# Kernel tuning notes

Measured on AMD Instinct MI355X. Metric: run time of the kernel, lower is better.

## Reference

```python
import jax, jax.numpy as jnp
import numpy as np

NUM_GROUPS = 32
EPS = 1e-6


def setup_inputs() -> dict:
    key = jax.random.key(0)
    ks = jax.random.split(key, 11)
    b, c, h, w = 4, 512, 64, 64
    s = 0.02
    return {
        "x": jax.random.normal(ks[0], (b, c, h, w), dtype=jnp.float32),
        "gn_w": jnp.ones((c,), dtype=jnp.float32),
        "gn_b": jnp.zeros((c,), dtype=jnp.float32),
        "wq": jax.random.normal(ks[1], (c, c), dtype=jnp.float32) * s,
        "bq": jax.random.normal(ks[2], (c,), dtype=jnp.float32) * s,
        "wk": jax.random.normal(ks[3], (c, c), dtype=jnp.float32) * s,
        "bk": jax.random.normal(ks[4], (c,), dtype=jnp.float32) * s,
        "wv": jax.random.normal(ks[5], (c, c), dtype=jnp.float32) * s,
        "bv": jax.random.normal(ks[6], (c,), dtype=jnp.float32) * s,
        "wo": jax.random.normal(ks[7], (c, c), dtype=jnp.float32) * s,
        "bo": jax.random.normal(ks[8], (c,), dtype=jnp.float32) * s,
    }


def _group_norm(x, gamma, beta):
    b, c, h, w = x.shape
    g = NUM_GROUPS
    xg = x.reshape(b, g, c // g, h, w)
    mean = jnp.mean(xg, axis=(2, 3, 4), keepdims=True)
    var = jnp.var(xg, axis=(2, 3, 4), keepdims=True)
    xg = (xg - mean) * jax.lax.rsqrt(var + EPS)
    x = xg.reshape(b, c, h, w)
    return x * gamma[None, :, None, None] + beta[None, :, None, None]


def _conv1x1(x, wmat, bias):
    # x: [b,c,h,w], wmat: [out,in] -> [b,out,h,w]
    return jnp.einsum('bchw,oc->bohw', x, wmat) + bias[None, :, None, None]


def reference(x, gn_w, gn_b, wq, bq, wk, bk, wv, bv, wo, bo):
    b, c, h, w = x.shape
    h_ = _group_norm(x, gn_w, gn_b)
    q = _conv1x1(h_, wq, bq).reshape(b, c, h * w)  # [b,c,hw]
    k = _conv1x1(h_, wk, bk).reshape(b, c, h * w)
    v = _conv1x1(h_, wv, bv).reshape(b, c, h * w)
    scale = float(c) ** (-0.5)
    # scores[b,i,j] = sum_c q[b,c,i] * k[b,c,j]
    scores = jnp.einsum('bci,bcj->bij', q, k) * scale
    attn = jax.nn.softmax(scores, axis=2)  # softmax over j (keys)
    # out[b,c,i] = sum_j v[b,c,j] * attn[b,i,j]
    out = jnp.einsum('bcj,bij->bci', v, attn).reshape(b, c, h, w)
    out = _conv1x1(out, wo, bo)
    return x + out
```

## Files before the change

### kernel.cpp

```cpp
#include <hip/hip_runtime.h>
#include <math.h>

using short8 = __attribute__((ext_vector_type(8))) short;
using f32x4  = __attribute__((ext_vector_type(4))) float;
using llong2 = __attribute__((ext_vector_type(2))) long long;
using i32x8  = __attribute__((ext_vector_type(8))) int;

__device__ __forceinline__ ushort f2bf(float f) {
    union { float f; uint u; } c; c.f = f;
    uint u = c.u;
    uint r = (u + 0x7FFFu + ((u >> 16) & 1u)) >> 16;
    return (ushort)r;
}
__device__ __forceinline__ float bf2f(ushort h) {
    union { uint u; float f; } c; c.u = ((uint)h) << 16;
    return c.f;
}
__device__ __forceinline__ uint pk4_fp8(float a, float b, float c, float d) {
    int v = __builtin_amdgcn_cvt_pk_fp8_f32(a, b, 0, false);
    v = __builtin_amdgcn_cvt_pk_fp8_f32(c, d, v, true);
    return (uint)v;
}
__device__ __forceinline__ unsigned char f2fp8(float x) {
    return (unsigned char)__builtin_amdgcn_cvt_pk_fp8_f32(x, 0.f, 0, false);
}

__device__ __forceinline__ void gload16(const void* g, void* l) {
    __builtin_amdgcn_global_load_lds(
        (const __attribute__((address_space(1))) unsigned int*)g,
        (__attribute__((address_space(3))) unsigned int*)l,
        16, 0, 0);
}

__global__ __launch_bounds__(256) void prep_weights(
    const float* __restrict__ wq, const float* __restrict__ bq,
    const float* __restrict__ wk, const float* __restrict__ bk,
    const float* __restrict__ wv, const float* __restrict__ wo,
    ushort* __restrict__ Wqk, ushort* __restrict__ Wv, ushort* __restrict__ Wo,
    float* __restrict__ bqk, float* __restrict__ stats, float scale)
{
    int idx = blockIdx.x * 256 + threadIdx.x;
    if (idx < 1024 * 512) {
        float v = (idx < 262144) ? wq[idx] * scale : wk[idx - 262144];
        Wqk[idx] = f2bf(v);
    }
    if (idx < 262144) {
        Wv[idx] = f2bf(wv[idx]);
        Wo[idx] = f2bf(wo[idx]);
    }
    if (idx < 1024) bqk[idx] = (idx < 512) ? bq[idx] * scale : bk[idx - 512];
    if (idx < 256) stats[idx] = 0.f;
}

__global__ __launch_bounds__(256) void gn_stats(
    const float* __restrict__ x, float* __restrict__ stats)
{
    int blk = blockIdx.x;
    int grp = blk >> 3, sub = blk & 7;
    const float* xp = x + (size_t)grp * 65536 + sub * 8192;
    int tid = threadIdx.x;

    float s = 0.f, sq = 0.f;
    #pragma unroll
    for (int j = 0; j < 8; ++j) {
        float4 v = *(const float4*)&xp[tid * 4 + j * 1024];
        s  += v.x + v.y + v.z + v.w;
        sq += v.x * v.x + v.y * v.y + v.z * v.z + v.w * v.w;
    }
    #pragma unroll
    for (int off = 32; off; off >>= 1) {
        s  += __shfl_xor(s,  off, 64);
        sq += __shfl_xor(sq, off, 64);
    }
    __shared__ float red[8];
    if ((tid & 63) == 0) { red[(tid >> 6) * 2] = s; red[(tid >> 6) * 2 + 1] = sq; }
    __syncthreads();
    if (tid == 0) {
        atomicAdd(&stats[grp * 2],     red[0] + red[2] + red[4] + red[6]);
        atomicAdd(&stats[grp * 2 + 1], red[1] + red[3] + red[5] + red[7]);
    }
}

__global__ __launch_bounds__(256) void gn_apply(
    const float* __restrict__ x, const float* __restrict__ gamma,
    const float* __restrict__ beta, const float* __restrict__ stats,
    ushort* __restrict__ hnt)
{
    int blk = blockIdx.x;
    int grp = blk >> 4, tile = blk & 15;
    int b = grp >> 5, g = grp & 31;
    const float* xp = x + (size_t)grp * 65536;
    int tid = threadIdx.x;

    float mean = stats[grp * 2] * (1.f / 65536.f);
    float var  = stats[grp * 2 + 1] * (1.f / 65536.f) - mean * mean;
    float rstd = rsqrtf(var + 1e-6f);

    int i0 = tile * 256;
    __shared__ ushort ls[16][256];
    #pragma unroll
    for (int ch = 0; ch < 16; ++ch) {
        float a = rstd * gamma[g * 16 + ch];
        float c = beta[g * 16 + ch] - mean * a;
        ls[ch][tid] = f2bf(xp[ch * 4096 + i0 + tid] * a + c);
    }
    __syncthreads();
    ushort t[16];
    #pragma unroll
    for (int ch = 0; ch < 16; ++ch) t[ch] = ls[ch][tid];
    size_t dst = ((size_t)b * 4096 + i0 + tid) * 512 + g * 16;
    *(uint4*)&hnt[dst]     = *(const uint4*)&t[0];
    *(uint4*)&hnt[dst + 8] = *(const uint4*)&t[8];
}

__global__ __launch_bounds__(256) void softmax_kernel(
    const ushort* __restrict__ S, unsigned char* __restrict__ P8)
{
    size_t row = blockIdx.x;
    const ushort* p = S + row * 4096;
    int tid = threadIdx.x;

    ushort tmp[16];
    *(uint4*)&tmp[0] = *(const uint4*)&p[tid * 16];
    *(uint4*)&tmp[8] = *(const uint4*)&p[tid * 16 + 8];
    float v[16];
    float mx = -1e30f;
    #pragma unroll
    for (int j = 0; j < 16; ++j) { v[j] = bf2f(tmp[j]); mx = fmaxf(mx, v[j]); }
    #pragma unroll
    for (int off = 32; off; off >>= 1) mx = fmaxf(mx, __shfl_xor(mx, off, 64));
    __shared__ float ls[8];
    if ((tid & 63) == 0) ls[tid >> 6] = mx;
    __syncthreads();
    float m4 = fmaxf(fmaxf(ls[0], ls[1]), fmaxf(ls[2], ls[3]));
    float sum = 0.f;
    #pragma unroll
    for (int j = 0; j < 16; ++j) { v[j] = __expf(v[j] - m4); sum += v[j]; }
    #pragma unroll
    for (int off = 32; off; off >>= 1) sum += __shfl_xor(sum, off, 64);
    if ((tid & 63) == 0) ls[4 + (tid >> 6)] = sum;
    __syncthreads();
    float inv = 256.0f / (ls[4] + ls[5] + ls[6] + ls[7]);
    size_t base = row * 4096 + (size_t)tid * 16;
    uint2 o0, o1;
    o0.x = pk4_fp8(v[0] * inv,  v[1] * inv,  v[2] * inv,  v[3] * inv);
    o0.y = pk4_fp8(v[4] * inv,  v[5] * inv,  v[6] * inv,  v[7] * inv);
    o1.x = pk4_fp8(v[8] * inv,  v[9] * inv,  v[10] * inv, v[11] * inv);
    o1.y = pk4_fp8(v[12] * inv, v[13] * inv, v[14] * inv, v[15] * inv);
    *(uint2*)&P8[base]     = o0;
    *(uint2*)&P8[base + 8] = o1;
}

template <int BIAS, int OUT>
__global__ __launch_bounds__(256, 4) void gemm_nt(
    const ushort* __restrict__ Ag, const ushort* __restrict__ Bg,
    void* __restrict__ Cv, void* __restrict__ Cv2,
    const float* __restrict__ bias, const float* __restrict__ resid,
    int N, int K, int lda, int ldb,
    long sA, long sB, long sC)
{
    const int bz = blockIdx.z;
    Ag += (size_t)bz * sA;
    Bg += (size_t)bz * sB;

    const int tid  = threadIdx.x;
    const int wave = tid >> 6, lane = tid & 63;
    const int q = lane >> 4, lr = lane & 15;
    const int m0 = blockIdx.x * 128, n0 = blockIdx.y * 128;
    const int wm = (wave >> 1) * 64, wn = (wave & 1) * 64;

    __shared__ __align__(16) ushort As[2][128 * 32];
    __shared__ __align__(16) ushort Bs[2][128 * 32];

    const int srow = wave * 32 + (lane >> 2);
    const int skc  = (lane & 3) << 3;
    const size_t aoff0 = (size_t)(m0 + srow) * lda + skc;
    const size_t aoff1 = aoff0 + (size_t)16 * lda;
    const size_t boff0 = (size_t)(n0 + srow) * ldb + skc;
    const size_t boff1 = boff0 + (size_t)16 * ldb;
    const int l0 = wave * 1024, l1 = wave * 1024 + 512;

    f32x4 acc[4][4] = {};

    for (int kb = 0; kb < K; kb += 64) {
        __syncthreads();
        gload16(&Ag[aoff0 + kb],      &As[0][l0]);
        gload16(&Ag[aoff1 + kb],      &As[0][l1]);
        gload16(&Ag[aoff0 + kb + 32], &As[1][l0]);
        gload16(&Ag[aoff1 + kb + 32], &As[1][l1]);
        gload16(&Bg[boff0 + kb],      &Bs[0][l0]);
        gload16(&Bg[boff1 + kb],      &Bs[0][l1]);
        gload16(&Bg[boff0 + kb + 32], &Bs[1][l0]);
        gload16(&Bg[boff1 + kb + 32], &Bs[1][l1]);
        __syncthreads();

        #pragma unroll
        for (int kh = 0; kh < 2; ++kh) {
            short8 af[4], bfr[4];
            #pragma unroll
            for (int mt = 0; mt < 4; ++mt)
                af[mt] = *(const short8*)&As[kh][(wm + mt * 16 + lr) * 32 + q * 8];
            #pragma unroll
            for (int nt = 0; nt < 4; ++nt)
                bfr[nt] = *(const short8*)&Bs[kh][(wn + nt * 16 + lr) * 32 + q * 8];
            #pragma unroll
            for (int mt = 0; mt < 4; ++mt)
                #pragma unroll
                for (int nt = 0; nt < 4; ++nt)
                    acc[mt][nt] = __builtin_amdgcn_mfma_f32_16x16x32_bf16(
                        af[mt], bfr[nt], acc[mt][nt], 0, 0, 0);
        }
    }

    #pragma unroll
    for (int mt = 0; mt < 4; ++mt) {
        int rb = m0 + wm + mt * 16 + q * 4;
        #pragma unroll
        for (int nt = 0; nt < 4; ++nt) {
            int cn = n0 + wn + nt * 16 + lr;
            #pragma unroll
            for (int t = 0; t < 4; ++t) {
                int r = rb + t;
                float v = acc[mt][nt][t];
                if (BIAS == 1) v += bias[r];
                if (BIAS == 2) v += bias[cn];
                if (OUT == 1) {
                    size_t o = (size_t)bz * sC + (size_t)r * N + cn;
                    ((float*)Cv)[o] = v + resid[o];
                } else if (OUT == 2) {
                    ((unsigned char*)Cv)[(size_t)bz * sC + (size_t)r * N + cn] =
                        f2fp8(v);
                } else if (OUT == 3) {
                    if (cn < 512)
                        ((unsigned char*)Cv)[(size_t)bz * sC + (size_t)r * 512 + cn]
                            = f2fp8(v * 16.f);
                    else
                        ((unsigned char*)Cv2)[(size_t)bz * sC + (size_t)r * 512 + (cn - 512)]
                            = f2fp8(v);
                } else {
                    size_t o = (size_t)bz * sC + (size_t)r * N + cn;
                    ((ushort*)Cv)[o] = f2bf(v);
                }
            }
        }
    }
}

__global__ __launch_bounds__(256, 2) void gemm_qk(
    const unsigned char* __restrict__ Q8, const unsigned char* __restrict__ K8,
    ushort* __restrict__ S)
{
    const int bz = blockIdx.z;
    const unsigned char* Ag = Q8 + (size_t)bz * 2097152;
    const unsigned char* Bg = K8 + (size_t)bz * 2097152;

    const int tid  = threadIdx.x;
    const int wave = tid >> 6, lane = tid & 63;
    const int q = lane >> 4, lr = lane & 15;
    const int m0 = blockIdx.x * 128, n0 = blockIdx.y * 128;
    const int wm = (wave >> 1) * 64, wn = (wave & 1) * 64;

    __shared__ __align__(16) unsigned char As[2][128 * 128];
    __shared__ __align__(16) unsigned char Bs[2][128 * 128];

    const int lrow = lane >> 3;
    const size_t laneoff = (size_t)lrow * 512 + ((lane & 7) ^ (lrow & 7)) * 16;
    const size_t abase = (size_t)(m0 + wave * 32) * 512 + laneoff;
    const size_t bbase = (size_t)(n0 + wave * 32) * 512 + laneoff;
    const int lbase = wave * 32 * 128;

    const int e0 = (2 * q) ^ (lr & 7), e1 = e0 ^ 1;

    f32x4 acc[4][4] = {};
    const int sA = 0x7B7B7B7B;
    const int sB = 0x7F7F7F7F;

    auto stage = [&](int kb, int buf) {
        #pragma unroll
        for (int t = 0; t < 4; ++t) {
            gload16(Ag + abase + (size_t)t * 4096 + kb, &As[buf][lbase + t * 1024]);
            gload16(Bg + bbase + (size_t)t * 4096 + kb, &Bs[buf][lbase + t * 1024]);
        }
    };

    stage(0, 0);
    __syncthreads();

    for (int it = 0; it < 4; ++it) {
        const int cur = it & 1;
        if (it < 3) stage((it + 1) * 128, cur ^ 1);

        i32x8 af[4], bf[4];
        #pragma unroll
        for (int mt = 0; mt < 4; ++mt) {
            int r = wm + mt * 16 + lr;
            union { uint4 v[2]; i32x8 f; } u;
            u.v[0] = *(const uint4*)&As[cur][r * 128 + e0 * 16];
            u.v[1] = *(const uint4*)&As[cur][r * 128 + e1 * 16];
            af[mt] = u.f;
        }
        #pragma unroll
        for (int nt = 0; nt < 4; ++nt) {
            int r = wn + nt * 16 + lr;
            union { uint4 v[2]; i32x8 f; } u;
            u.v[0] = *(const uint4*)&Bs[cur][r * 128 + e0 * 16];
            u.v[1] = *(const uint4*)&Bs[cur][r * 128 + e1 * 16];
            bf[nt] = u.f;
        }
        #pragma unroll
        for (int mt = 0; mt < 4; ++mt)
            #pragma unroll
            for (int nt = 0; nt < 4; ++nt)
                acc[mt][nt] = __builtin_amdgcn_mfma_scale_f32_16x16x128_f8f6f4(
                    af[mt], bf[nt], acc[mt][nt], 0, 0, 0, sA, 0, sB);

        __syncthreads();
    }

    #pragma unroll
    for (int mt = 0; mt < 4; ++mt) {
        int rb = m0 + wm + mt * 16 + q * 4;
        #pragma unroll
        for (int nt = 0; nt < 4; ++nt) {
            int cn = n0 + wn + nt * 16 + lr;
            #pragma unroll
            for (int t = 0; t < 4; ++t) {
                size_t o = (size_t)bz * 16777216 + (size_t)(rb + t) * 4096 + cn;
                S[o] = f2bf(acc[mt][nt][t]);
            }
        }
    }
}

__global__ __launch_bounds__(256, 2) void gemm_pv(
    const unsigned char* __restrict__ P8, const unsigned char* __restrict__ V8,
    ushort* __restrict__ Ot)
{
    const int bz = blockIdx.z;
    const unsigned char* Ag = P8 + (size_t)bz * 16777216;
    const unsigned char* Bg = V8 + (size_t)bz * 2097152;

    const int tid  = threadIdx.x;
    const int wave = tid >> 6, lane = tid & 63;
    const int q = lane >> 4, lr = lane & 15;
    const int m0 = blockIdx.x * 128, n0 = blockIdx.y * 128;
    const int wm = (wave >> 1) * 64, wn = (wave & 1) * 64;

    __shared__ __align__(16) unsigned char As[2][128 * 128];
    __shared__ __align__(16) unsigned char Bs[2][128 * 128];

    const int lrow = lane >> 3;
    const size_t laneoff = (size_t)lrow * 4096 + ((lane & 7) ^ (lrow & 7)) * 16;
    const size_t abase = (size_t)(m0 + wave * 32) * 4096 + laneoff;
    const size_t bbase = (size_t)(n0 + wave * 32) * 4096 + laneoff;
    const int lbase = wave * 32 * 128;

    const int e0 = (2 * q) ^ (lr & 7), e1 = e0 ^ 1;

    f32x4 acc[4][4] = {};
    const int sA = 0x77777777;
    const int sB = 0x7F7F7F7F;

    auto stage = [&](int kb, int buf) {
        #pragma unroll
        for (int t = 0; t < 4; ++t) {
            gload16(Ag + abase + (size_t)t * 32768 + kb, &As[buf][lbase + t * 1024]);
            gload16(Bg + bbase + (size_t)t * 32768 + kb, &Bs[buf][lbase + t * 1024]);
        }
    };

    stage(0, 0);
    __syncthreads();

    for (int it = 0; it < 32; ++it) {
        const int cur = it & 1;
        if (it < 31) stage((it + 1) * 128, cur ^ 1);

        i32x8 af[4], bf[4];
        #pragma unroll
        for (int mt = 0; mt < 4; ++mt) {
            int r = wm + mt * 16 + lr;
            union { uint4 v[2]; i32x8 f; } u;
            u.v[0] = *(const uint4*)&As[cur][r * 128 + e0 * 16];
            u.v[1] = *(const uint4*)&As[cur][r * 128 + e1 * 16];
            af[mt] = u.f;
        }
        #pragma unroll
        for (int nt = 0; nt < 4; ++nt) {
            int r = wn + nt * 16 + lr;
            union { uint4 v[2]; i32x8 f; } u;
            u.v[0] = *(const uint4*)&Bs[cur][r * 128 + e0 * 16];
            u.v[1] = *(const uint4*)&Bs[cur][r * 128 + e1 * 16];
            bf[nt] = u.f;
        }
        #pragma unroll
        for (int mt = 0; mt < 4; ++mt)
            #pragma unroll
            for (int nt = 0; nt < 4; ++nt)
                acc[mt][nt] = __builtin_amdgcn_mfma_scale_f32_16x16x128_f8f6f4(
                    af[mt], bf[nt], acc[mt][nt], 0, 0, 0, sA, 0, sB);

        __syncthreads();
    }

    #pragma unroll
    for (int mt = 0; mt < 4; ++mt) {
        int rb = m0 + wm + mt * 16 + q * 4;
        #pragma unroll
        for (int nt = 0; nt < 4; ++nt) {
            int cn = n0 + wn + nt * 16 + lr;
            #pragma unroll
            for (int t = 0; t < 4; ++t) {
                size_t o = (size_t)bz * 2097152 + (size_t)(rb + t) * 512 + cn;
                Ot[o] = f2bf(acc[mt][nt][t]);
            }
        }
    }
}

extern "C" void kernel_launch(void* const* d_in, const int* in_sizes, int n_in,
                              void* d_out, int out_size, void* d_ws, size_t ws_size,
                              hipStream_t stream)
{
    const float* x   = (const float*)d_in[0];
    const float* gnw = (const float*)d_in[1];
    const float* gnb = (const float*)d_in[2];
    const float* wq  = (const float*)d_in[3];
    const float* bq  = (const float*)d_in[4];
    const float* wk  = (const float*)d_in[5];
    const float* bk  = (const float*)d_in[6];
    const float* wv  = (const float*)d_in[7];
    const float* bv  = (const float*)d_in[8];
    const float* wo  = (const float*)d_in[9];
    const float* bo  = (const float*)d_in[10];
    float* out = (float*)d_out;

    char* ws = (char*)d_ws;
    ushort*        S   = (ushort*)(ws);
    ushort*        Ot  = (ushort*)(ws);
    ushort*        hnt = (ushort*)(ws + 134217728);
    unsigned char* Q8  = (unsigned char*)(ws + 150994944);
    unsigned char* K8  = (unsigned char*)(ws + 159383552);
    unsigned char* P8  = (unsigned char*)(ws + 134217728);
    unsigned char* V8  = (unsigned char*)(ws + 201326592);
    ushort*        Wqk = (ushort*)(ws + 209715200);
    ushort*        Wv  = (ushort*)(ws + 210763776);
    ushort*        Wo  = (ushort*)(ws + 211288064);
    float*         bqk = (float*) (ws + 211812352);
    float*         st  = (float*) (ws + 211816448);

    const float scale = 1.0f / sqrtf(512.0f);
    const long sHW  = 512L * 4096;

    prep_weights<<<2048, 256, 0, stream>>>(wq, bq, wk, bk, wv, wo,
                                           Wqk, Wv, Wo, bqk, st, scale);
    gn_stats<<<1024, 256, 0, stream>>>(x, st);
    gn_apply<<<2048, 256, 0, stream>>>(x, gnw, gnb, st, hnt);

    gemm_nt<2, 3><<<dim3(32, 8, 4), 256, 0, stream>>>(
        hnt, Wqk, Q8, K8, bqk, nullptr,
        1024, 512, 512, 512, sHW, 0L, sHW);

    gemm_nt<1, 2><<<dim3(4, 32, 4), 256, 0, stream>>>(
        Wv, hnt, V8, nullptr, bv, nullptr,
        4096, 512, 512, 512, 0L, sHW, sHW);

    gemm_qk<<<dim3(32, 32, 4), 256, 0, stream>>>(Q8, K8, S);

    softmax_kernel<<<16384, 256, 0, stream>>>(S, P8);

    gemm_pv<<<dim3(32, 4, 4), 256, 0, stream>>>(P8, V8, Ot);

    gemm_nt<1, 1><<<dim3(4, 32, 4), 256, 0, stream>>>(
        Wo, Ot, out, nullptr, bo, x,
        4096, 512, 512, 512, 0L, sHW, sHW);
}
```

Measured before the change: 301.9 us.

## Stage GEMM epilogues through LDS for coalesced 16-byte stores, single-buffer fp8 GEMMs

The fp8 projection outputs and the QK/PV GEMM bf16 outputs are now written into a swizzled shared-memory tile first, then stored to global memory as 16-byte vector rows instead of scattered 1- or 2-byte stores. This targets uncoalesced write traffic, which matters most for the large bf16 score matrix. To make room in LDS, gemm_qk and gemm_pv drop double buffering and go to a single 32KB buffer with two barriers per k-step. That halves LDS use and may raise occupancy, but loads no longer overlap with MFMA work inside a block.

After: 285.5 us. 1.06x faster.

```diff
diff --git a/kernel.cpp b/kernel.cpp
--- a/kernel.cpp
+++ b/kernel.cpp
@@ -212,6 +212,47 @@
         }
     }
 
+    if (OUT == 2 || OUT == 3) {
+        __syncthreads();
+        unsigned char* C8 = (unsigned char*)&As[0][0];
+        #pragma unroll
+        for (int mt = 0; mt < 4; ++mt) {
+            #pragma unroll
+            for (int nt = 0; nt < 4; ++nt) {
+                int col = wn + nt * 16 + lr;
+                #pragma unroll
+                for (int t = 0; t < 4; ++t) {
+                    int row = wm + mt * 16 + q * 4 + t;
+                    float v = acc[mt][nt][t];
+                    if (BIAS == 1) v += bias[m0 + row];
+                    if (BIAS == 2) v += bias[n0 + col];
+                    if (OUT == 3 && n0 < 512) v *= 16.f;
+                    C8[row * 128 + ((((col >> 4) ^ (row & 7)) << 4) | (col & 15))]
+                        = f2fp8(v);
+                }
+            }
+        }
+        __syncthreads();
+        const int er = tid >> 3, eck = tid & 7;
+        #pragma unroll
+        for (int p = 0; p < 4; ++p) {
+            int row = p * 32 + er;
+            uint4 v = *(const uint4*)&C8[row * 128 + ((eck ^ (row & 7)) << 4)];
+            if (OUT == 2) {
+                *(uint4*)&((unsigned char*)Cv)[(size_t)bz * sC
+                    + (size_t)(m0 + row) * N + n0 + eck * 16] = v;
+            } else {
+                if (n0 < 512)
+                    *(uint4*)&((unsigned char*)Cv)[(size_t)bz * sC
+                        + (size_t)(m0 + row) * 512 + n0 + eck * 16] = v;
+                else
+                    *(uint4*)&((unsigned char*)Cv2)[(size_t)bz * sC
+                        + (size_t)(m0 + row) * 512 + (n0 - 512) + eck * 16] = v;
+            }
+        }
+        return;
+    }
+
     #pragma unroll
     for (int mt = 0; mt < 4; ++mt) {
         int rb = m0 + wm + mt * 16 + q * 4;
@@ -227,16 +268,6 @@
                 if (OUT == 1) {
                     size_t o = (size_t)bz * sC + (size_t)r * N + cn;
                     ((float*)Cv)[o] = v + resid[o];
-                } else if (OUT == 2) {
-                    ((unsigned char*)Cv)[(size_t)bz * sC + (size_t)r * N + cn] =
-                        f2fp8(v);
-                } else if (OUT == 3) {
-                    if (cn < 512)
-                        ((unsigned char*)Cv)[(size_t)bz * sC + (size_t)r * 512 + cn]
-                            = f2fp8(v * 16.f);
-                    else
-                        ((unsigned char*)Cv2)[(size_t)bz * sC + (size_t)r * 512 + (cn - 512)]
-                            = f2fp8(v);
                 } else {
                     size_t o = (size_t)bz * sC + (size_t)r * N + cn;
                     ((ushort*)Cv)[o] = f2bf(v);
@@ -260,14 +291,17 @@
     const int m0 = blockIdx.x * 128, n0 = blockIdx.y * 128;
     const int wm = (wave >> 1) * 64, wn = (wave & 1) * 64;
 
-    __shared__ __align__(16) unsigned char As[2][128 * 128];
-    __shared__ __align__(16) unsigned char Bs[2][128 * 128];
+    __shared__ __align__(16) unsigned char smem[32768];
+    unsigned char* As = smem;
+    unsigned char* Bs = smem + 16384;
+    ushort* Cs = (ushort*)smem;
 
     const int lrow = lane >> 3;
     const size_t laneoff = (size_t)lrow * 512 + ((lane & 7) ^ (lrow & 7)) * 16;
     const size_t abase = (size_t)(m0 + wave * 32) * 512 + laneoff;
     const size_t bbase = (size_t)(n0 + wave * 32) * 512 + laneoff;
-    const int lbase = wave * 32 * 128;
+    unsigned char* lA = As + wave * 32 * 128;
+    unsigned char* lB = Bs + wave * 32 * 128;
 
     const int e0 = (2 * q) ^ (lr & 7), e1 = e0 ^ 1;
 
@@ -275,36 +309,30 @@
     const int sA = 0x7B7B7B7B;
     const int sB = 0x7F7F7F7F;
 
-    auto stage = [&](int kb, int buf) {
+    for (int kb = 0; kb < 512; kb += 128) {
+        __syncthreads();
         #pragma unroll
         for (int t = 0; t < 4; ++t) {
-            gload16(Ag + abase + (size_t)t * 4096 + kb, &As[buf][lbase + t * 1024]);
-            gload16(Bg + bbase + (size_t)t * 4096 + kb, &Bs[buf][lbase + t * 1024]);
-        }
-    };
-
-    stage(0, 0);
-    __syncthreads();
-
-    for (int it = 0; it < 4; ++it) {
-        const int cur = it & 1;
-        if (it < 3) stage((it + 1) * 128, cur ^ 1);
+            gload16(Ag + abase + (size_t)t * 4096 + kb, lA + t * 1024);
+            gload16(Bg + bbase + (size_t)t * 4096 + kb, lB + t * 1024);
+        }
+        __syncthreads();
 
         i32x8 af[4], bf[4];
         #pragma unroll
         for (int mt = 0; mt < 4; ++mt) {
             int r = wm + mt * 16 + lr;
             union { uint4 v[2]; i32x8 f; } u;
-            u.v[0] = *(const uint4*)&As[cur][r * 128 + e0 * 16];
-            u.v[1] = *(const uint4*)&As[cur][r * 128 + e1 * 16];
+            u.v[0] = *(const uint4*)&As[r * 128 + e0 * 16];
+            u.v[1] = *(const uint4*)&As[r * 128 + e1 * 16];
             af[mt] = u.f;
         }
         #pragma unroll
         for (int nt = 0; nt < 4; ++nt) {
             int r = wn + nt * 16 + lr;
             union { uint4 v[2]; i32x8 f; } u;
-            u.v[0] = *(const uint4*)&Bs[cur][r * 128 + e0 * 16];
-            u.v[1] = *(const uint4*)&Bs[cur][r * 128 + e1 * 16];
+            u.v[0] = *(const uint4*)&Bs[r * 128 + e0 * 16];
+            u.v[1] = *(const uint4*)&Bs[r * 128 + e1 * 16];
             bf[nt] = u.f;
         }
         #pragma unroll
@@ -313,22 +341,30 @@
             for (int nt = 0; nt < 4; ++nt)
                 acc[mt][nt] = __builtin_amdgcn_mfma_scale_f32_16x16x128_f8f6f4(
                     af[mt], bf[nt], acc[mt][nt], 0, 0, 0, sA, 0, sB);
-
-        __syncthreads();
-    }
-
+    }
+
+    __syncthreads();
     #pragma unroll
     for (int mt = 0; mt < 4; ++mt) {
-        int rb = m0 + wm + mt * 16 + q * 4;
         #pragma unroll
         for (int nt = 0; nt < 4; ++nt) {
-            int cn = n0 + wn + nt * 16 + lr;
+            int col = wn + nt * 16 + lr;
             #pragma unroll
             for (int t = 0; t < 4; ++t) {
-                size_t o = (size_t)bz * 16777216 + (size_t)(rb + t) * 4096 + cn;
-                S[o] = f2bf(acc[mt][nt][t]);
+                int row = wm + mt * 16 + q * 4 + t;
+                Cs[row * 128 + ((((col >> 3) ^ (row & 7)) << 3) | (col & 7))]
+                    = f2bf(acc[mt][nt][t]);
             }
         }
+    }
+    __syncthreads();
+    const int er = tid >> 4, eck = tid & 15;
+    ushort* orow = S + (size_t)bz * 16777216 + (size_t)m0 * 4096 + n0;
+    #pragma unroll
+    for (int p = 0; p < 8; ++p) {
+        int row = p * 16 + er;
+        uint4 v = *(const uint4*)&Cs[row * 128 + ((eck ^ (row & 7)) << 3)];
+        *(uint4*)&orow[(size_t)row * 4096 + eck * 8] = v;
     }
 }
 
@@ -346,14 +382,17 @@
     const int m0 = blockIdx.x * 128, n0 = blockIdx.y * 128;
     const int wm = (wave >> 1) * 64, wn = (wave & 1) * 64;
 
-    __shared__ __align__(16) unsigned char As[2][128 * 128];
-    __shared__ __align__(16) unsigned char Bs[2][128 * 128];
+    __shared__ __align__(16) unsigned char smem[32768];
+    unsigned char* As = smem;
+    unsigned char* Bs = smem + 16384;
+    ushort* Cs = (ushort*)smem;
 
     const int lrow = lane >> 3;
     const size_t laneoff = (size_t)lrow * 4096 + ((lane & 7) ^ (lrow & 7)) * 16;
     const size_t abase = (size_t)(m0 + wave * 32) * 4096 + laneoff;
     const size_t bbase = (size_t)(n0 + wave * 32) * 4096 + laneoff;
-    const int lbase = wave * 32 * 128;
+    unsigned char* lA = As + wave * 32 * 128;
+    unsigned char* lB = Bs + wave * 32 * 128;
 
     const int e0 = (2 * q) ^ (lr & 7), e1 = e0 ^ 1;
 
@@ -361,36 +400,30 @@
     const int sA = 0x77777777;
     const int sB = 0x7F7F7F7F;
 
-    auto stage = [&](int kb, int buf) {
+    for (int kb = 0; kb < 4096; kb += 128) {
+        __syncthreads();
         #pragma unroll
         for (int t = 0; t < 4; ++t) {
-            gload16(Ag + abase + (size_t)t * 32768 + kb, &As[buf][lbase + t * 1024]);
-            gload16(Bg + bbase + (size_t)t * 32768 + kb, &Bs[buf][lbase + t * 1024]);
-        }
-    };
-
-    stage(0, 0);
-    __syncthreads();
-
-    for (int it = 0; it < 32; ++it) {
-        const int cur = it & 1;
-        if (it < 31) stage((it + 1) * 128, cur ^ 1);
+            gload16(Ag + abase + (size_t)t * 32768 + kb, lA + t * 1024);
+            gload16(Bg + bbase + (size_t)t * 32768 + kb, lB + t * 1024);
+        }
+        __syncthreads();
 
         i32x8 af[4], bf[4];
         #pragma unroll
         for (int mt = 0; mt < 4; ++mt) {
             int r = wm + mt * 16 + lr;
             union { uint4 v[2]; i32x8 f; } u;
-            u.v[0] = *(const uint4*)&As[cur][r * 128 + e0 * 16];
-            u.v[1] = *(const uint4*)&As[cur][r * 128 + e1 * 16];
+            u.v[0] = *(const uint4*)&As[r * 128 + e0 * 16];
+            u.v[1] = *(const uint4*)&As[r * 128 + e1 * 16];
             af[mt] = u.f;
         }
         #pragma unroll
         for (int nt = 0; nt < 4; ++nt) {
             int r = wn + nt * 16 + lr;
             union { uint4 v[2]; i32x8 f; } u;
-            u.v[0] = *(const uint4*)&Bs[cur][r * 128 + e0 * 16];
-            u.v[1] = *(const uint4*)&Bs[cur][r * 128 + e1 * 16];
+            u.v[0] = *(const uint4*)&Bs[r * 128 + e0 * 16];
+            u.v[1] = *(const uint4*)&Bs[r * 128 + e1 * 16];
             bf[nt] = u.f;
         }
         #pragma unroll
@@ -399,22 +432,30 @@
             for (int nt = 0; nt < 4; ++nt)
                 acc[mt][nt] = __builtin_amdgcn_mfma_scale_f32_16x16x128_f8f6f4(
                     af[mt], bf[nt], acc[mt][nt], 0, 0, 0, sA, 0, sB);
-
-        __syncthreads();
-    }
-
+    }
+
+    __syncthreads();
     #pragma unroll
     for (int mt = 0; mt < 4; ++mt) {
-        int rb = m0 + wm + mt * 16 + q * 4;
         #pragma unroll
         for (int nt = 0; nt < 4; ++nt) {
-            int cn = n0 + wn + nt * 16 + lr;
+            int col = wn + nt * 16 + lr;
             #pragma unroll
             for (int t = 0; t < 4; ++t) {
-                size_t o = (size_t)bz * 2097152 + (size_t)(rb + t) * 512 + cn;
-                Ot[o] = f2bf(acc[mt][nt][t]);
+                int row = wm + mt * 16 + q * 4 + t;
+                Cs[row * 128 + ((((col >> 3) ^ (row & 7)) << 3) | (col & 7))]
+                    = f2bf(acc[mt][nt][t]);
             }
         }
+    }
+    __syncthreads();
+    const int er = tid >> 4, eck = tid & 15;
+    ushort* orow = Ot + (size_t)bz * 2097152 + (size_t)m0 * 512 + n0;
+    #pragma unroll
+    for (int p = 0; p < 8; ++p) {
+        int row = p * 16 + er;
+        uint4 v = *(const uint4*)&Cs[row * 128 + ((eck ^ (row & 7)) << 3)];
+        *(uint4*)&orow[(size_t)row * 512 + eck * 8] = v;
     }
 }
 
```
